# Optimization experiments

Measured on AMD Instinct MI355X. Metric: run time of the kernel, lower is better.

Reference implementation:

```python
import jax, jax.numpy as jnp
import numpy as np

N_NODES = 100000
N_EDGES = 640000
IN_DIM = 128
OUT_DIM = 128
EDGE_DIM = 4
N_GROUPS = 8
EPS = 1e-5


def setup_inputs() -> dict:
    key = jax.random.key(0)
    ks = jax.random.split(key, 9)
    x = jax.random.normal(ks[0], (N_NODES, IN_DIM), dtype=jnp.float32)
    edge_index = jax.random.randint(ks[1], (2, N_EDGES), 0, N_NODES, dtype=jnp.int64)
    edge_attr = jax.random.normal(ks[2], (N_EDGES, EDGE_DIM), dtype=jnp.float32)
    d_in = 2 * IN_DIM + EDGE_DIM
    # Linear layers (kaiming-uniform-ish init scale)
    W1 = jax.random.uniform(ks[3], (d_in, OUT_DIM), jnp.float32, -1, 1) / np.sqrt(d_in)
    b1 = jax.random.uniform(ks[4], (OUT_DIM,), jnp.float32, -1, 1) / np.sqrt(d_in)
    W2 = jax.random.uniform(ks[5], (OUT_DIM, OUT_DIM), jnp.float32, -1, 1) / np.sqrt(OUT_DIM)
    b2 = jax.random.uniform(ks[6], (OUT_DIM,), jnp.float32, -1, 1) / np.sqrt(OUT_DIM)
    gn_gamma = jnp.ones((OUT_DIM,), jnp.float32)
    gn_beta = jnp.zeros((OUT_DIM,), jnp.float32)
    return {"x": x, "edge_index": edge_index, "edge_attr": edge_attr,
            "W1": W1, "b1": b1, "gn_gamma": gn_gamma, "gn_beta": gn_beta,
            "W2": W2, "b2": b2}


def group_norm(h, gamma, beta):
    # h: [E, C]; normalize each row per group of C//N_GROUPS channels
    E, C = h.shape
    hg = h.reshape(E, N_GROUPS, C // N_GROUPS)
    mean = jnp.mean(hg, axis=-1, keepdims=True)
    var = jnp.mean(jnp.square(hg - mean), axis=-1, keepdims=True)
    hg = (hg - mean) * jax.lax.rsqrt(var + EPS)
    return hg.reshape(E, C) * gamma + beta


def reference(x, edge_index, edge_attr, W1, b1, gn_gamma, gn_beta, W2, b2):
    src, dst = edge_index[0], edge_index[1]
    # gather endpoint features: [E, 2*in_dim + edge_dim]
    feat = jnp.concatenate([x[dst], x[src], edge_attr], axis=-1)
    h = feat @ W1 + b1                      # [E, out_dim]
    h = group_norm(h, gn_gamma, gn_beta)
    h = jax.nn.silu(h)
    messages = h @ W2 + b2                  # [E, out_dim]
    out = jax.ops.segment_sum(messages, dst, num_segments=x.shape[0])
    count = jax.ops.segment_sum(jnp.ones((messages.shape[0], 1), x.dtype), dst,
                                num_segments=x.shape[0])
    return out / jnp.maximum(count, 1.0)
```

## Files before the change

### kernel.cpp

```cpp
#include <hip/hip_runtime.h>
#include <hip/hip_bf16.h>

#define NNODES 100000
#define NEDGES 640000
#define DIM 128
#define GS 16
#define EB 64
#define NSCAN_BLOCKS ((NNODES + 255) / 256)
#define G1_BLOCKS ((NNODES + 63) / 64)

typedef __attribute__((ext_vector_type(8))) short short8;
typedef __attribute__((ext_vector_type(4))) float f32x4;

__device__ __forceinline__ ushort f2bf(float f) {
    __hip_bfloat16 h = __float2bfloat16(f);
    return *reinterpret_cast<ushort*>(&h);
}
__device__ __forceinline__ float bf2f(ushort u) {
    union { unsigned int i; float f; } v; v.i = ((unsigned int)u) << 16; return v.f;
}

__global__ void zero_kernel(float* __restrict__ out, int* __restrict__ hist) {
    long step = (long)gridDim.x * blockDim.x;
    long i0 = (long)blockIdx.x * blockDim.x + threadIdx.x;
    const long total = (long)NNODES * DIM;
    for (long i = i0; i < total; i += step) out[i] = 0.f;
    for (long i = i0; i < NNODES; i += step) hist[i] = 0;
}

__global__ __launch_bounds__(256) void node_gemm1(const float* __restrict__ x,
                                                  const float* __restrict__ W1,
                                                  ushort* __restrict__ xab) {
    __shared__ __align__(16) char xt[64 * 256];
    const int tid  = threadIdx.x;
    const int lane = tid & 63;
    const int w    = tid >> 6;
    const int lr   = lane & 15;
    const int lg   = lane >> 4;
    const int m0   = blockIdx.x * 64;
    const int mtMax = (m0 + 64 <= NNODES) ? 4 : 2;

    const int koff = (w >= 2) ? 128 : 0;
    short8 bfrag[4][4];
    #pragma unroll
    for (int nt = 0; nt < 4; ++nt) {
        const int cc = (w & 1) * 64 + nt * 16 + lr;
        #pragma unroll
        for (int kt = 0; kt < 4; ++kt) {
            const int kb = koff + kt * 32 + lg * 8;
            short8 f;
            #pragma unroll
            for (int j = 0; j < 8; ++j) f[j] = (short)f2bf(W1[(long)(kb + j) * DIM + cc]);
            bfrag[nt][kt] = f;
        }
    }

    {
        const int r  = tid >> 2;
        const int kq = (tid & 3) * 32;
        if (m0 + r < NNODES) {
            const float* xr = &x[(long)(m0 + r) * DIM + kq];
            ushort tmp[32];
            #pragma unroll
            for (int j = 0; j < 32; ++j) tmp[j] = f2bf(xr[j]);
            #pragma unroll
            for (int i = 0; i < 4; ++i) {
                int byte = r * 256 + kq * 2 + i * 16;
                byte ^= (r & 7) << 4;
                *(short8*)(xt + byte) = *(short8*)&tmp[i * 8];
            }
        }
    }
    __syncthreads();

    const int colBase = w * 64;
    for (int mt = 0; mt < mtMax; ++mt) {
        short8 afrag[4];
        #pragma unroll
        for (int kt = 0; kt < 4; ++kt) {
            const int row = mt * 16 + lr;
            int byte = row * 256 + (kt * 4 + lg) * 16;
            byte ^= (row & 7) << 4;
            afrag[kt] = *(short8*)(xt + byte);
        }
        f32x4 acc[4] = {};
        #pragma unroll
        for (int nt = 0; nt < 4; ++nt)
            #pragma unroll
            for (int kt = 0; kt < 4; ++kt)
                acc[nt] = __builtin_amdgcn_mfma_f32_16x16x32_bf16(afrag[kt], bfrag[nt][kt], acc[nt], 0, 0, 0);
        #pragma unroll
        for (int nt = 0; nt < 4; ++nt) {
            const int col = colBase + nt * 16 + lr;
            #pragma unroll
            for (int r = 0; r < 4; ++r) {
                const int row = m0 + mt * 16 + lg * 4 + r;
                xab[(long)row * 256 + col] = f2bf(acc[nt][r]);
            }
        }
    }
}

__global__ void hist_kernel(const int* __restrict__ ei, int* __restrict__ hist) {
    int e = blockIdx.x * 256 + threadIdx.x;
    if (e < NEDGES) atomicAdd(&hist[ei[NEDGES + e]], 1);
}

__global__ void scan1_kernel(const int* __restrict__ hist, int* __restrict__ excl,
                             int* __restrict__ bsums) {
    __shared__ int s[256];
    int tid = threadIdx.x;
    int i = blockIdx.x * 256 + tid;
    int v = (i < NNODES) ? hist[i] : 0;
    s[tid] = v;
    __syncthreads();
    for (int o = 1; o < 256; o <<= 1) {
        int t = (tid >= o) ? s[tid - o] : 0;
        __syncthreads();
        s[tid] += t;
        __syncthreads();
    }
    if (i < NNODES) excl[i] = s[tid] - v;
    if (tid == 255) bsums[blockIdx.x] = s[255];
}

__global__ void scan2_kernel(int* __restrict__ bsums) {
    __shared__ int s[512];
    int tid = threadIdx.x;
    int v = (tid < NSCAN_BLOCKS) ? bsums[tid] : 0;
    s[tid] = v;
    __syncthreads();
    for (int o = 1; o < 512; o <<= 1) {
        int t = (tid >= o) ? s[tid - o] : 0;
        __syncthreads();
        s[tid] += t;
        __syncthreads();
    }
    if (tid < NSCAN_BLOCKS) bsums[tid] = s[tid] - v;
}

__global__ void scan3_kernel(const int* __restrict__ excl, const int* __restrict__ bsums,
                             int* __restrict__ cursor) {
    int i = blockIdx.x * 256 + threadIdx.x;
    if (i < NNODES) cursor[i] = excl[i] + bsums[blockIdx.x];
}

__global__ void scatter_kernel(const int* __restrict__ ei, int* __restrict__ cursor,
                               int* __restrict__ sorted) {
    int e = blockIdx.x * 256 + threadIdx.x;
    if (e < NEDGES) {
        int d = ei[NEDGES + e];
        int pos = atomicAdd(&cursor[d], 1);
        sorted[pos] = e;
    }
}

__global__ __launch_bounds__(256) void edge_silu_kernel(
    const ushort* __restrict__ xab,
    const int* __restrict__ ei, const float* __restrict__ ea,
    const int* __restrict__ sorted,
    const float* __restrict__ W1, const float* __restrict__ b1,
    const float* __restrict__ gamma, const float* __restrict__ beta,
    float* __restrict__ out)
{
    __shared__ __align__(16) ushort ssilu[EB * 128];
    __shared__ __align__(16) float4 w1ct[132];
    __shared__ float sbb1[132], sgam[132], sbet[132];
    __shared__ int   sdst[EB], ssrc[EB];
    __shared__ float4 sea4[EB];

    const int tid = threadIdx.x;
    const int e0 = blockIdx.x * EB;

    if (tid < EB) {
        int id = sorted[e0 + tid];
        sdst[tid] = ei[NEDGES + id];
        ssrc[tid] = ei[id];
        sea4[tid] = *(const float4*)&ea[(long)id * 4];
    }
    if (tid < 128) {
        int c = tid;
        int p = c + (c >> 5);
        w1ct[p] = make_float4(W1[256 * DIM + c], W1[257 * DIM + c],
                              W1[258 * DIM + c], W1[259 * DIM + c]);
        sbb1[p] = b1[c]; sgam[p] = gamma[c]; sbet[p] = beta[c];
    }
    __syncthreads();

    {
        const int e = tid >> 2;
        const int q = tid & 3;
        const int c0 = q * 32;
        const int pBase = c0 + q;
        const ushort* xaRow = &xab[(long)sdst[e] * 256 + c0];
        const ushort* xbRow = &xab[(long)ssrc[e] * 256 + 128 + c0];
        const float4 a = sea4[e];

        float v[32];
        #pragma unroll
        for (int i = 0; i < 4; ++i) {
            short8 ga = *(const short8*)&xaRow[i * 8];
            short8 gb = *(const short8*)&xbRow[i * 8];
            #pragma unroll
            for (int j = 0; j < 8; ++j) {
                const int idx = i * 8 + j;
                const float4 w = w1ct[pBase + idx];
                float t = sbb1[pBase + idx] + a.x * w.x + a.y * w.y + a.z * w.z + a.w * w.w;
                v[idx] = t + bf2f((ushort)ga[j]) + bf2f((ushort)gb[j]);
            }
        }

        #pragma unroll
        for (int g = 0; g < 2; ++g) {
            float s = 0.f, qq = 0.f;
            #pragma unroll
            for (int i = 0; i < GS; ++i) {
                float a2 = v[g * GS + i];
                s += a2; qq += a2 * a2;
            }
            const float m = s * (1.f / GS);
            const float var = qq * (1.f / GS) - m * m;
            const float inv = rsqrtf(var + 1e-5f);
            #pragma unroll
            for (int i = 0; i < GS; ++i) {
                const int idx = g * GS + i;
                const float sc = sgam[pBase + idx] * inv;
                const float off = sbet[pBase + idx] - m * sc;
                float t = v[idx] * sc + off;
                v[idx] = t / (1.f + __expf(-t));
            }
        }

        ushort tmp[32];
        #pragma unroll
        for (int j = 0; j < 32; ++j) tmp[j] = f2bf(v[j]);
        #pragma unroll
        for (int i = 0; i < 4; ++i) {
            int byte = (e * 256 + (c0 + i * 8) * 2) ^ ((e & 7) << 4);
            *(short8*)((char*)ssilu + byte) = *(short8*)&tmp[i * 8];
        }
    }
    __syncthreads();

    {
        const int c = tid & 127;
        const int h = tid >> 7;
        const int eS = h * 32, eE = eS + 32;
        float r = 0.f;
        int cur = sdst[eS];
        for (int ee = eS; ee < eE; ++ee) {
            int d = sdst[ee];
            if (d != cur) {
                unsafeAtomicAdd(&out[(long)cur * DIM + c], r);
                r = 0.f; cur = d;
            }
            int byte = (ee * 256 + c * 2) ^ ((ee & 7) << 4);
            r += bf2f(*(const ushort*)((const char*)ssilu + byte));
        }
        unsafeAtomicAdd(&out[(long)cur * DIM + c], r);
    }
}

__global__ __launch_bounds__(256) void node_gemm2(float* __restrict__ out,
                                                  const float* __restrict__ W2,
                                                  const float* __restrict__ b2,
                                                  const int* __restrict__ hist) {
    __shared__ __align__(16) char at[64 * 256];
    __shared__ float sb2[128];
    __shared__ int scnt[64];
    const int tid  = threadIdx.x;
    const int lane = tid & 63;
    const int w    = tid >> 6;
    const int lr   = lane & 15;
    const int lg   = lane >> 4;
    const int m0   = blockIdx.x * 64;
    const int mtMax = (m0 + 64 <= NNODES) ? 4 : 2;

    short8 bfrag[2][4];
    #pragma unroll
    for (int nt = 0; nt < 2; ++nt) {
        const int cc = w * 32 + nt * 16 + lr;
        #pragma unroll
        for (int kt = 0; kt < 4; ++kt) {
            const int kb = kt * 32 + lg * 8;
            short8 f;
            #pragma unroll
            for (int j = 0; j < 8; ++j) f[j] = (short)f2bf(W2[(long)(kb + j) * DIM + cc]);
            bfrag[nt][kt] = f;
        }
    }

    if (tid < 128) sb2[tid] = b2[tid];
    if (tid < 64 && m0 + tid < NNODES) scnt[tid] = hist[m0 + tid];

    {
        const int r  = tid >> 2;
        const int kq = (tid & 3) * 32;
        if (m0 + r < NNODES) {
            const float* ar = &out[(long)(m0 + r) * DIM + kq];
            ushort tmp[32];
            #pragma unroll
            for (int j = 0; j < 32; ++j) tmp[j] = f2bf(ar[j]);
            #pragma unroll
            for (int i = 0; i < 4; ++i) {
                int byte = r * 256 + kq * 2 + i * 16;
                byte ^= (r & 7) << 4;
                *(short8*)(at + byte) = *(short8*)&tmp[i * 8];
            }
        }
    }
    __syncthreads();

    for (int mt = 0; mt < mtMax; ++mt) {
        short8 afrag[4];
        #pragma unroll
        for (int kt = 0; kt < 4; ++kt) {
            const int row = mt * 16 + lr;
            int byte = row * 256 + (kt * 4 + lg) * 16;
            byte ^= (row & 7) << 4;
            afrag[kt] = *(short8*)(at + byte);
        }
        f32x4 acc[2] = {};
        #pragma unroll
        for (int nt = 0; nt < 2; ++nt)
            #pragma unroll
            for (int kt = 0; kt < 4; ++kt)
                acc[nt] = __builtin_amdgcn_mfma_f32_16x16x32_bf16(afrag[kt], bfrag[nt][kt], acc[nt], 0, 0, 0);
        #pragma unroll
        for (int nt = 0; nt < 2; ++nt) {
            const int col = w * 32 + nt * 16 + lr;
            #pragma unroll
            for (int r = 0; r < 4; ++r) {
                const int rr = mt * 16 + lg * 4 + r;
                float cnt = (float)scnt[rr];
                float sc = 1.f / fmaxf(cnt, 1.f);
                out[(long)(m0 + rr) * DIM + col] = (acc[nt][r] + cnt * sb2[col]) * sc;
            }
        }
    }
}

extern "C" void kernel_launch(void* const* d_in, const int* in_sizes, int n_in,
                              void* d_out, int out_size, void* d_ws, size_t ws_size,
                              hipStream_t stream) {
    const float* x     = (const float*)d_in[0];
    const int*   ei    = (const int*)  d_in[1];
    const float* ea    = (const float*)d_in[2];
    const float* W1    = (const float*)d_in[3];
    const float* b1    = (const float*)d_in[4];
    const float* gamma = (const float*)d_in[5];
    const float* beta  = (const float*)d_in[6];
    const float* W2    = (const float*)d_in[7];
    const float* b2    = (const float*)d_in[8];
    float* out = (float*)d_out;

    char* ws = (char*)d_ws;
    size_t off = 0;
    ushort* xab   = (ushort*)(ws + off); off += (size_t)NNODES * 256 * sizeof(ushort);
    int*    hist  = (int*)   (ws + off); off += (size_t)NNODES * sizeof(int);
    int*    excl  = (int*)   (ws + off); off += (size_t)NNODES * sizeof(int);
    int*    cursor= (int*)   (ws + off); off += (size_t)NNODES * sizeof(int);
    int*    bsums = (int*)   (ws + off); off += 512 * sizeof(int);
    int*    sorted= (int*)   (ws + off); off += (size_t)NEDGES * sizeof(int);

    zero_kernel<<<2048, 256, 0, stream>>>(out, hist);
    node_gemm1<<<G1_BLOCKS, 256, 0, stream>>>(x, W1, xab);
    hist_kernel<<<(NEDGES + 255) / 256, 256, 0, stream>>>(ei, hist);
    scan1_kernel<<<NSCAN_BLOCKS, 256, 0, stream>>>(hist, excl, bsums);
    scan2_kernel<<<1, 512, 0, stream>>>(bsums);
    scan3_kernel<<<NSCAN_BLOCKS, 256, 0, stream>>>(excl, bsums, cursor);
    scatter_kernel<<<(NEDGES + 255) / 256, 256, 0, stream>>>(ei, cursor, sorted);
    edge_silu_kernel<<<NEDGES / EB, 256, 0, stream>>>(xab, ei, ea, sorted,
                                                      W1, b1, gamma, beta, out);
    node_gemm2<<<G1_BLOCKS, 256, 0, stream>>>(out, W2, b2, hist);
}
```

Measured before the change: 228.2 us.

## Pre-sort edge endpoints and attributes in scatter, fold b1 into node GEMM

The scatter pass now writes the (dst, src) pairs and edge attributes directly in dst-sorted order. This removes the indirect gather through the sorted index array in the edge kernel. The b1 bias is folded into the node GEMM1 output, and the per-edge SiLU results are kept in fp32 shared memory with float4-vectorised segmented reduction over 8-edge runs. Fast rcp/rsq intrinsics replace divisions. In exchange it adds extra workspace writes in scatter, doubles the LDS footprint, and issues more atomics because the reduction runs are shorter.

```diff
diff --git a/kernel.cpp b/kernel.cpp
--- a/kernel.cpp
+++ b/kernel.cpp
@@ -30,6 +30,7 @@
 
 __global__ __launch_bounds__(256) void node_gemm1(const float* __restrict__ x,
                                                   const float* __restrict__ W1,
+                                                  const float* __restrict__ b1,
                                                   ushort* __restrict__ xab) {
     __shared__ __align__(16) char xt[64 * 256];
     const int tid  = threadIdx.x;
@@ -92,10 +93,11 @@
         #pragma unroll
         for (int nt = 0; nt < 4; ++nt) {
             const int col = colBase + nt * 16 + lr;
+            const float badd = (koff == 0) ? b1[col] : 0.f;
             #pragma unroll
             for (int r = 0; r < 4; ++r) {
                 const int row = m0 + mt * 16 + lg * 4 + r;
-                xab[(long)row * 256 + col] = f2bf(acc[nt][r]);
+                xab[(long)row * 256 + col] = f2bf(acc[nt][r] + badd);
             }
         }
     }
@@ -145,45 +147,44 @@
     if (i < NNODES) cursor[i] = excl[i] + bsums[blockIdx.x];
 }
 
-__global__ void scatter_kernel(const int* __restrict__ ei, int* __restrict__ cursor,
-                               int* __restrict__ sorted) {
+__global__ void scatter_kernel(const int* __restrict__ ei, const float* __restrict__ ea,
+                               int* __restrict__ cursor,
+                               int2* __restrict__ dstsrc, float4* __restrict__ eas) {
     int e = blockIdx.x * 256 + threadIdx.x;
     if (e < NEDGES) {
         int d = ei[NEDGES + e];
         int pos = atomicAdd(&cursor[d], 1);
-        sorted[pos] = e;
+        dstsrc[pos] = make_int2(d, ei[e]);
+        eas[pos] = *(const float4*)&ea[(long)e * 4];
     }
 }
 
 __global__ __launch_bounds__(256) void edge_silu_kernel(
     const ushort* __restrict__ xab,
-    const int* __restrict__ ei, const float* __restrict__ ea,
-    const int* __restrict__ sorted,
-    const float* __restrict__ W1, const float* __restrict__ b1,
+    const int2* __restrict__ dstsrc, const float4* __restrict__ eas,
+    const float* __restrict__ W1,
     const float* __restrict__ gamma, const float* __restrict__ beta,
     float* __restrict__ out)
 {
-    __shared__ __align__(16) ushort ssilu[EB * 128];
+    __shared__ __align__(16) float ssilu[EB * 128];
     __shared__ __align__(16) float4 w1ct[132];
-    __shared__ float sbb1[132], sgam[132], sbet[132];
-    __shared__ int   sdst[EB], ssrc[EB];
+    __shared__ __align__(8)  float2 gbt[132];
+    __shared__ int2   sds[EB];
     __shared__ float4 sea4[EB];
 
     const int tid = threadIdx.x;
     const int e0 = blockIdx.x * EB;
 
     if (tid < EB) {
-        int id = sorted[e0 + tid];
-        sdst[tid] = ei[NEDGES + id];
-        ssrc[tid] = ei[id];
-        sea4[tid] = *(const float4*)&ea[(long)id * 4];
+        sds[tid]  = dstsrc[e0 + tid];
+        sea4[tid] = eas[e0 + tid];
     }
     if (tid < 128) {
         int c = tid;
         int p = c + (c >> 5);
         w1ct[p] = make_float4(W1[256 * DIM + c], W1[257 * DIM + c],
                               W1[258 * DIM + c], W1[259 * DIM + c]);
-        sbb1[p] = b1[c]; sgam[p] = gamma[c]; sbet[p] = beta[c];
+        gbt[p] = make_float2(gamma[c], beta[c]);
     }
     __syncthreads();
 
@@ -192,8 +193,9 @@
         const int q = tid & 3;
         const int c0 = q * 32;
         const int pBase = c0 + q;
-        const ushort* xaRow = &xab[(long)sdst[e] * 256 + c0];
-        const ushort* xbRow = &xab[(long)ssrc[e] * 256 + 128 + c0];
+        const int2 ds = sds[e];
+        const ushort* xaRow = &xab[(long)ds.x * 256 + c0];
+        const ushort* xbRow = &xab[(long)ds.y * 256 + 128 + c0];
         const float4 a = sea4[e];
 
         float v[32];
@@ -205,7 +207,8 @@
             for (int j = 0; j < 8; ++j) {
                 const int idx = i * 8 + j;
                 const float4 w = w1ct[pBase + idx];
-                float t = sbb1[pBase + idx] + a.x * w.x + a.y * w.y + a.z * w.z + a.w * w.w;
+                float t = a.x * w.x + a.y * w.y;
+                t += a.z * w.z + a.w * w.w;
                 v[idx] = t + bf2f((ushort)ga[j]) + bf2f((ushort)gb[j]);
             }
         }
@@ -220,44 +223,52 @@
             }
             const float m = s * (1.f / GS);
             const float var = qq * (1.f / GS) - m * m;
-            const float inv = rsqrtf(var + 1e-5f);
+            const float inv = __builtin_amdgcn_rsqf(var + 1e-5f);
             #pragma unroll
             for (int i = 0; i < GS; ++i) {
                 const int idx = g * GS + i;
-                const float sc = sgam[pBase + idx] * inv;
-                const float off = sbet[pBase + idx] - m * sc;
+                const float2 gb2 = gbt[pBase + idx];
+                const float sc = gb2.x * inv;
+                const float off = gb2.y - m * sc;
                 float t = v[idx] * sc + off;
-                v[idx] = t / (1.f + __expf(-t));
-            }
-        }
-
-        ushort tmp[32];
-        #pragma unroll
-        for (int j = 0; j < 32; ++j) tmp[j] = f2bf(v[j]);
-        #pragma unroll
-        for (int i = 0; i < 4; ++i) {
-            int byte = (e * 256 + (c0 + i * 8) * 2) ^ ((e & 7) << 4);
-            *(short8*)((char*)ssilu + byte) = *(short8*)&tmp[i * 8];
+                v[idx] = t * __builtin_amdgcn_rcpf(1.f + __expf(-t));
+            }
+        }
+
+        #pragma unroll
+        for (int i = 0; i < 8; ++i) {
+            const int c4 = q * 8 + i;
+            const int pos = c4 ^ (e & 7);
+            *(float4*)&ssilu[e * 128 + pos * 4] = make_float4(v[i*4+0], v[i*4+1], v[i*4+2], v[i*4+3]);
         }
     }
     __syncthreads();
 
     {
-        const int c = tid & 127;
-        const int h = tid >> 7;
-        const int eS = h * 32, eE = eS + 32;
-        float r = 0.f;
-        int cur = sdst[eS];
+        const int c4 = tid & 31;
+        const int seg = tid >> 5;
+        const int eS = seg * 8, eE = eS + 8;
+        float4 r = make_float4(0.f, 0.f, 0.f, 0.f);
+        int cur = sds[eS].x;
         for (int ee = eS; ee < eE; ++ee) {
-            int d = sdst[ee];
+            int d = sds[ee].x;
             if (d != cur) {
-                unsafeAtomicAdd(&out[(long)cur * DIM + c], r);
-                r = 0.f; cur = d;
-            }
-            int byte = (ee * 256 + c * 2) ^ ((ee & 7) << 4);
-            r += bf2f(*(const ushort*)((const char*)ssilu + byte));
-        }
-        unsafeAtomicAdd(&out[(long)cur * DIM + c], r);
+                long base = (long)cur * DIM + c4 * 4;
+                unsafeAtomicAdd(&out[base + 0], r.x);
+                unsafeAtomicAdd(&out[base + 1], r.y);
+                unsafeAtomicAdd(&out[base + 2], r.z);
+                unsafeAtomicAdd(&out[base + 3], r.w);
+                r = make_float4(0.f, 0.f, 0.f, 0.f);
+                cur = d;
+            }
+            const float4 s = *(const float4*)&ssilu[ee * 128 + (c4 ^ (ee & 7)) * 4];
+            r.x += s.x; r.y += s.y; r.z += s.z; r.w += s.w;
+        }
+        long base = (long)cur * DIM + c4 * 4;
+        unsafeAtomicAdd(&out[base + 0], r.x);
+        unsafeAtomicAdd(&out[base + 1], r.y);
+        unsafeAtomicAdd(&out[base + 2], r.z);
+        unsafeAtomicAdd(&out[base + 3], r.w);
     }
 }
 
@@ -333,7 +344,7 @@
             for (int r = 0; r < 4; ++r) {
                 const int rr = mt * 16 + lg * 4 + r;
                 float cnt = (float)scnt[rr];
-                float sc = 1.f / fmaxf(cnt, 1.f);
+                float sc = __builtin_amdgcn_rcpf(fmaxf(cnt, 1.f));
                 out[(long)(m0 + rr) * DIM + col] = (acc[nt][r] + cnt * sb2[col]) * sc;
             }
         }
@@ -361,16 +372,18 @@
     int*    excl  = (int*)   (ws + off); off += (size_t)NNODES * sizeof(int);
     int*    cursor= (int*)   (ws + off); off += (size_t)NNODES * sizeof(int);
     int*    bsums = (int*)   (ws + off); off += 512 * sizeof(int);
-    int*    sorted= (int*)   (ws + off); off += (size_t)NEDGES * sizeof(int);
+    int2*   dstsrc= (int2*)  (ws + off); off += (size_t)NEDGES * sizeof(int2);
+    off = (off + 15) & ~(size_t)15;
+    float4* eas   = (float4*)(ws + off); off += (size_t)NEDGES * sizeof(float4);
 
     zero_kernel<<<2048, 256, 0, stream>>>(out, hist);
-    node_gemm1<<<G1_BLOCKS, 256, 0, stream>>>(x, W1, xab);
+    node_gemm1<<<G1_BLOCKS, 256, 0, stream>>>(x, W1, b1, xab);
     hist_kernel<<<(NEDGES + 255) / 256, 256, 0, stream>>>(ei, hist);
     scan1_kernel<<<NSCAN_BLOCKS, 256, 0, stream>>>(hist, excl, bsums);
     scan2_kernel<<<1, 512, 0, stream>>>(bsums);
     scan3_kernel<<<NSCAN_BLOCKS, 256, 0, stream>>>(excl, bsums, cursor);
-    scatter_kernel<<<(NEDGES + 255) / 256, 256, 0, stream>>>(ei, cursor, sorted);
-    edge_silu_kernel<<<NEDGES / EB, 256, 0, stream>>>(xab, ei, ea, sorted,
-                                                      W1, b1, gamma, beta, out);
+    scatter_kernel<<<(NEDGES + 255) / 256, 256, 0, stream>>>(ei, ea, cursor, dstsrc, eas);
+    edge_silu_kernel<<<NEDGES / EB, 256, 0, stream>>>(xab, dstsrc, eas,
+                                                      W1, gamma, beta, out);
     node_gemm2<<<G1_BLOCKS, 256, 0, stream>>>(out, W2, b2, hist);
 }
```

Result: slower. 437.0 us (+91.5%).
